# Performance work log

Measured on AMD Instinct MI355X. Metric: run time of the kernel, lower is better.

Reference implementation:

```python
import jax, jax.numpy as jnp
import numpy as np

B, S, D_MODEL = 2, 8192, 768
NUM_HEADS = 12
R = 4          # dilation_rate (= number of independent attention branches)
SEG = 512      # segment_size


def setup_inputs() -> dict:
    key = jax.random.key(0)
    ks = jax.random.split(key, 3)
    x = jax.random.normal(ks[0], (B, S, D_MODEL), jnp.float32)
    # Per-offset MHA weights: fused qkv proj and output proj (bias zeros)
    Wqkv = jax.random.normal(ks[1], (R, 3 * D_MODEL, D_MODEL), jnp.float32) * 0.02
    bqkv = jnp.zeros((R, 3 * D_MODEL), jnp.float32)
    Wout = jax.random.normal(ks[2], (R, D_MODEL, D_MODEL), jnp.float32) * 0.02
    bout = jnp.zeros((R, D_MODEL), jnp.float32)
    return {"x": x, "Wqkv": Wqkv, "bqkv": bqkv, "Wout": Wout, "bout": bout,
            "num_heads": NUM_HEADS}


def reference(x, Wqkv, bqkv, Wout, bout, num_heads):
    Bb, Ss, D = x.shape
    r = Wqkv.shape[0]
    L = Ss // r                # tokens per dilation offset
    n_seg = L // SEG           # segments per offset
    hd = D // num_heads

    # Dilated strided gather: x[:, o::r, :] for all offsets o -> (r, B, L, D)
    xo = jnp.moveaxis(x.reshape(Bb, L, r, D), 2, 0)

    # Per-offset fused qkv projection
    qkv = jnp.einsum('rbld,red->rble', xo, Wqkv) + bqkv[:, None, None, :]
    q, k, v = jnp.split(qkv, 3, axis=-1)
    seg = lambda t: t.reshape(r, Bb, n_seg, SEG, num_heads, hd)
    q, k, v = seg(q), seg(k), seg(v)  # (r, B, n_seg, SEG, H, hd)

    scale = 1.0 / np.sqrt(hd).astype(np.float32)
    scores = jnp.einsum('rbnqhd,rbnkhd->rbnhqk', q, k) * scale
    attn = jax.nn.softmax(scores, axis=-1)
    ctx = jnp.einsum('rbnhqk,rbnkhd->rbnqhd', attn, v).reshape(r, Bb, L, D)

    # Per-offset output projection
    out = jnp.einsum('rbld,red->rble', ctx, Wout) + bout[:, None, None, :]  # (r,B,L,D)

    # Scatter each offset's output back to its strided positions, zeros elsewhere,
    # then concat over offsets along the feature dim -> (B, S, r*D)
    res = jnp.zeros((Bb, Ss, r * D), x.dtype)
    for o in range(r):  # fixed small loop over dilation offsets
        res = res.at[:, o::r, o * D:(o + 1) * D].set(out[o])
    return res
```

## Files before the change

### kernel.cpp

```cpp
#include <hip/hip_runtime.h>

constexpr int Bb   = 2;
constexpr int S    = 8192;
constexpr int D    = 768;
constexpr int H    = 12;
constexpr int HD   = 64;
constexpr int R    = 4;
constexpr int L    = 2048;
constexpr int SEG  = 512;
constexpr int NSEG = 4;
constexpr int E3   = 3 * D;
constexpr int RD   = R * D;

typedef _Float16 f16x8 __attribute__((ext_vector_type(8)));
typedef _Float16 f16x4 __attribute__((ext_vector_type(4)));
typedef float    f32x4 __attribute__((ext_vector_type(4)));

#define AS1 __attribute__((address_space(1)))
#define AS3 __attribute__((address_space(3)))

__device__ __forceinline__ void gld16(const void* g, void* l) {
    __builtin_amdgcn_global_load_lds((AS1 void*)g, (AS3 void*)l, 16, 0, 0);
}

__global__ __launch_bounds__(256) void conv_one(const float4* __restrict__ x,
                                                f16x4* __restrict__ o, int n4)
{
    int i = blockIdx.x * 256 + threadIdx.x;
    const int stride = gridDim.x * 256;
    for (; i < n4; i += stride) {
        float4 v = x[i];
        f16x4 h;
        h[0] = (_Float16)v.x; h[1] = (_Float16)v.y;
        h[2] = (_Float16)v.z; h[3] = (_Float16)v.w;
        o[i] = h;
    }
}

template <int MODE>
__global__ __launch_bounds__(256) void mfma_gemm(const _Float16* __restrict__ Ah0,
                                                 const _Float16* __restrict__ Wh0,
                                                 const float* __restrict__ B0,
                                                 _Float16* __restrict__ Q0,
                                                 _Float16* __restrict__ K0,
                                                 _Float16* __restrict__ V0,
                                                 float* __restrict__ C0)
{
    constexpr int NXB = (MODE == 0) ? 18 : 6;
    constexpr int NWG = NXB * 16 * 8;
    const int wg = ((int)blockIdx.x & 7) * (NWG >> 3) + ((int)blockIdx.x >> 3);
    const int n0 = (wg % NXB) * 128;
    const int m0 = ((wg / NXB) & 15) * 128;
    const int z  = wg / (NXB * 16);
    const int r = z >> 1, b = z & 1;

    const _Float16* Ah; const _Float16* Wh; const float* bias;
    int lda;
    if (MODE == 0) {
        Ah = Ah0 + ((size_t)b * S + r) * D;  lda = RD;
        Wh = Wh0 + (size_t)r * E3 * D;
        bias = B0 + r * E3;
    } else {
        Ah = Ah0 + (size_t)z * L * D;        lda = D;
        Wh = Wh0 + (size_t)r * D * D;
        bias = B0 + r * D;
    }

    const int tid  = threadIdx.x;
    const int wave = tid >> 6;
    const int lane = tid & 63;
    const int lw   = lane & 15;
    const int quad = lane >> 4;
    const int wm   = wave & 1, wn = wave >> 1;

    __shared__ _Float16 sm[3][2][4096];

    f32x4 acc[4][4];
    #pragma unroll
    for (int mt = 0; mt < 4; mt++)
        #pragma unroll
        for (int nt = 0; nt < 4; nt++)
            acc[mt][nt] = f32x4{0.f, 0.f, 0.f, 0.f};

    const int srow = lane & 15;
    const int scol = (lane >> 4) * 8;

    auto stage = [&](int buf, int k0) {
        #pragma unroll
        for (int i = 0; i < 4; i++) {
            const int idx  = wave * 4 + i;
            const int tile = idx >> 3, g = idx & 7;
            const _Float16* src = (tile == 0) ? Ah : Wh;
            const int ldr   = (tile == 0) ? lda : D;
            const int base0 = (tile == 0) ? m0 : n0;
            gld16(src + (size_t)(base0 + g * 16 + srow) * ldr + k0 + scol,
                  &sm[buf][tile][g * 512]);
        }
    };

    stage(0, 0);
    stage(1, 32);

    for (int k = 0; k < 24; k++) {
        asm volatile("s_waitcnt lgkmcnt(0)" ::: "memory");
        if (k == 23) asm volatile("s_waitcnt vmcnt(0)" ::: "memory");
        else         asm volatile("s_waitcnt vmcnt(4)" ::: "memory");
        __builtin_amdgcn_s_barrier();
        __builtin_amdgcn_sched_barrier(0);

        const int buf = k % 3;
        f16x8 af[4], bf[4];
        #pragma unroll
        for (int mt = 0; mt < 4; mt++)
            af[mt] = *(const f16x8*)&sm[buf][0][(wm * 4 + mt) * 512 + quad * 128 + lw * 8];
        #pragma unroll
        for (int nt = 0; nt < 4; nt++)
            bf[nt] = *(const f16x8*)&sm[buf][1][(wn * 4 + nt) * 512 + quad * 128 + lw * 8];
        if (k + 2 < 24) stage((k + 2) % 3, (k + 2) * 32);
        #pragma unroll
        for (int mt = 0; mt < 4; mt++)
            #pragma unroll
            for (int nt = 0; nt < 4; nt++)
                acc[mt][nt] = __builtin_amdgcn_mfma_f32_16x16x32_f16(af[mt], bf[nt], acc[mt][nt], 0, 0, 0);
    }
    __syncthreads();

    float bv[4];
    #pragma unroll
    for (int nt = 0; nt < 4; nt++)
        bv[nt] = bias[n0 + wn * 64 + nt * 16 + lw];

    if (MODE == 0) {
        const int reg = n0 / D;
        if (reg < 2) {
            _Float16* G = (reg == 0 ? Q0 : K0) + (size_t)z * L * D;
            const int colbase = (n0 - reg * D) + wn * 64;
            _Float16* wbuf = &sm[0][0][wave * 2048];
            #pragma unroll
            for (int p = 0; p < 2; p++) {
                #pragma unroll
                for (int mtl = 0; mtl < 2; mtl++) {
                    const int mt = p * 2 + mtl;
                    #pragma unroll
                    for (int nt = 0; nt < 4; nt++)
                        #pragma unroll
                        for (int rr = 0; rr < 4; rr++)
                            wbuf[(mtl * 16 + quad * 4 + rr) * 64 + nt * 16 + lw] =
                                (_Float16)(acc[mt][nt][rr] + bv[nt]);
                }
                asm volatile("s_waitcnt lgkmcnt(0)" ::: "memory");
                #pragma unroll
                for (int j = 0; j < 4; j++) {
                    const int rl = (lane >> 3) + j * 8;
                    f16x8 v = *(const f16x8*)&wbuf[rl * 64 + (lane & 7) * 8];
                    const int l = m0 + wm * 64 + p * 32 + rl;
                    *(f16x8*)(G + (size_t)l * D + colbase + (lane & 7) * 8) = v;
                }
                asm volatile("s_waitcnt lgkmcnt(0)" ::: "memory");
            }
        } else {
            #pragma unroll
            for (int nt = 0; nt < 4; nt++) {
                const int e  = (n0 - 2 * D) + wn * 64 + nt * 16 + lw;
                const int hh = e >> 6, hd = e & 63;
                #pragma unroll
                for (int mt = 0; mt < 4; mt++) {
                    const int l = m0 + wm * 64 + mt * 16 + quad * 4;
                    const int ns = l >> 9, key = l & 511;
                    f16x4 v;
                    #pragma unroll
                    for (int rr = 0; rr < 4; rr++)
                        v[rr] = (_Float16)(acc[mt][nt][rr] + bv[nt]);
                    *(f16x4*)(V0 + ((size_t)((z * H + hh) * NSEG + ns)) * (HD * SEG)
                              + (size_t)hd * SEG + key) = v;
                }
            }
        }
    } else {
        float* Crow = C0 + (size_t)b * S * RD;
        #pragma unroll
        for (int mt = 0; mt < 4; mt++)
            #pragma unroll
            for (int nt = 0; nt < 4; nt++) {
                const int col = n0 + wn * 64 + nt * 16 + lw;
                #pragma unroll
                for (int rr = 0; rr < 4; rr++) {
                    const int l = m0 + wm * 64 + mt * 16 + quad * 4 + rr;
                    const float val = acc[mt][nt][rr] + bv[nt];
                    const size_t rowoff = (size_t)(l * R + r) * RD;
                    #pragma unroll
                    for (int rp = 0; rp < 4; rp++)
                        Crow[rowoff + rp * D + col] = (rp == r) ? val : 0.f;
                }
            }
    }
}

__global__ __launch_bounds__(256) void attn_mfma(const _Float16* __restrict__ Qh,
                                                 const _Float16* __restrict__ Kh,
                                                 const _Float16* __restrict__ Vt,
                                                 _Float16* __restrict__ ctx)
{
    __shared__ _Float16 Ks[3][4096];
    __shared__ _Float16 Vs[3][4096];
    __shared__ _Float16 Pw[16384];

    int t = ((int)blockIdx.x & 7) * 96 + ((int)blockIdx.x >> 3);
    const int qh = t & 1; t >>= 1;
    const int h  = t % H; t /= H;
    const int n  = t & 3; t >>= 2;
    const int z  = t;

    const int tid  = threadIdx.x;
    const int wave = tid >> 6;
    const int lane = tid & 63;
    const int lw   = lane & 15;
    const int quad = lane >> 4;
    const int srow = lane & 15;
    const int scol = (lane >> 4) * 8;

    const _Float16* Qg = Qh + ((size_t)(z * L + n * SEG + qh * 256)) * D + h * HD;
    #pragma unroll
    for (int i = 0; i < 8; i++) {
        const int qg = wave * 4 + (i >> 1), h2 = i & 1;
        gld16(Qg + (size_t)(qg * 16 + srow) * D + h2 * 32 + scol,
              &Pw[qg * 1024 + h2 * 512]);
    }
    __syncthreads();

    f16x8 qf[4][2];
    #pragma unroll
    for (int mt = 0; mt < 4; mt++)
        #pragma unroll
        for (int kk = 0; kk < 2; kk++)
            qf[mt][kk] = *(const f16x8*)&Pw[(wave * 4 + mt) * 1024 + (kk * 4 + quad) * 128 + lw * 8];

    const _Float16* Kg = Kh + ((size_t)(z * L + n * SEG)) * D + h * HD;
    const _Float16* Vg = Vt + ((size_t)((z * H + h) * NSEG + n)) * (HD * SEG);
    _Float16* Pv = Pw + wave * 4096;

    auto stageKV = [&](int buf, int kt) {
        #pragma unroll
        for (int i = 0; i < 4; i++) {
            const int idx = wave * 4 + i;
            const int j = idx & 7, g = j >> 1, h2 = j & 1;
            if (idx < 8)
                gld16(Kg + (size_t)(kt * 64 + g * 16 + srow) * D + h2 * 32 + scol,
                      &Ks[buf][g * 1024 + h2 * 512]);
            else
                gld16(Vg + (size_t)(g * 16 + srow) * SEG + kt * 64 + h2 * 32 + scol,
                      &Vs[buf][g * 1024 + h2 * 512]);
        }
    };

    f32x4 cacc[4][4];
    #pragma unroll
    for (int mt = 0; mt < 4; mt++)
        #pragma unroll
        for (int nt = 0; nt < 4; nt++)
            cacc[mt][nt] = f32x4{0.f, 0.f, 0.f, 0.f};
    float psum[4] = {0.f, 0.f, 0.f, 0.f};

    stageKV(0, 0);
    stageKV(1, 1);

    for (int kt = 0; kt < 8; kt++) {
        asm volatile("s_waitcnt lgkmcnt(0)" ::: "memory");
        if (kt == 7) asm volatile("s_waitcnt vmcnt(0)" ::: "memory");
        else         asm volatile("s_waitcnt vmcnt(4)" ::: "memory");
        __builtin_amdgcn_s_barrier();
        __builtin_amdgcn_sched_barrier(0);

        const int buf = kt % 3;
        if (kt + 2 < 8) stageKV((kt + 2) % 3, kt + 2);

        f32x4 Sc[4][4];
        #pragma unroll
        for (int mt = 0; mt < 4; mt++)
            #pragma unroll
            for (int nt = 0; nt < 4; nt++)
                Sc[mt][nt] = f32x4{0.f, 0.f, 0.f, 0.f};
        #pragma unroll
        for (int kk = 0; kk < 2; kk++)
            #pragma unroll
            for (int nt = 0; nt < 4; nt++) {
                f16x8 kf = *(const f16x8*)&Ks[buf][nt * 1024 + (kk * 4 + quad) * 128 + lw * 8];
                #pragma unroll
                for (int mt = 0; mt < 4; mt++)
                    Sc[mt][nt] = __builtin_amdgcn_mfma_f32_16x16x32_f16(kf, qf[mt][kk], Sc[mt][nt], 0, 0, 0);
            }

        #pragma unroll
        for (int mt = 0; mt < 4; mt++)
            #pragma unroll
            for (int nt = 0; nt < 4; nt++) {
                f16x4 p4;
                #pragma unroll
                for (int rr = 0; rr < 4; rr++)
                    p4[rr] = (_Float16)__expf(Sc[mt][nt][rr] * 0.125f);
                *(f16x4*)&Pv[mt * 1024 + (nt * 2 + (quad >> 1)) * 128 + lw * 8 + (quad & 1) * 4] = p4;
            }
        asm volatile("s_waitcnt lgkmcnt(0)" ::: "memory");

        #pragma unroll
        for (int kk = 0; kk < 2; kk++) {
            f16x8 pf[4], vf[4];
            #pragma unroll
            for (int mt = 0; mt < 4; mt++) {
                pf[mt] = *(const f16x8*)&Pv[mt * 1024 + (kk * 4 + quad) * 128 + lw * 8];
                float s = 0.f;
                #pragma unroll
                for (int j = 0; j < 8; j++) s += (float)pf[mt][j];
                psum[mt] += s;
            }
            #pragma unroll
            for (int nt = 0; nt < 4; nt++)
                vf[nt] = *(const f16x8*)&Vs[buf][nt * 1024 + (kk * 4 + quad) * 128 + lw * 8];
            #pragma unroll
            for (int mt = 0; mt < 4; mt++)
                #pragma unroll
                for (int nt = 0; nt < 4; nt++)
                    cacc[mt][nt] = __builtin_amdgcn_mfma_f32_16x16x32_f16(pf[mt], vf[nt], cacc[mt][nt], 0, 0, 0);
        }
    }

    #pragma unroll
    for (int mt = 0; mt < 4; mt++) {
        psum[mt] += __shfl_xor(psum[mt], 16);
        psum[mt] += __shfl_xor(psum[mt], 32);
    }
    _Float16* Cg = ctx + ((size_t)(z * L + n * SEG + qh * 256 + wave * 64)) * D + h * HD;
    #pragma unroll
    for (int mt = 0; mt < 4; mt++)
        #pragma unroll
        for (int rr = 0; rr < 4; rr++) {
            float iv = 1.0f / __shfl(psum[mt], quad * 4 + rr);
            int q = mt * 16 + quad * 4 + rr;
            #pragma unroll
            for (int nt = 0; nt < 4; nt++)
                Cg[(size_t)q * D + nt * 16 + lw] = (_Float16)(cacc[mt][nt][rr] * iv);
        }
}

extern "C" void kernel_launch(void* const* d_in, const int* in_sizes, int n_in,
                              void* d_out, int out_size, void* d_ws, size_t ws_size,
                              hipStream_t stream)
{
    const float* x    = (const float*)d_in[0];
    const float* Wqkv = (const float*)d_in[1];
    const float* bqkv = (const float*)d_in[2];
    const float* Wout = (const float*)d_in[3];
    const float* bout = (const float*)d_in[4];

    float* out = (float*)d_out;

    constexpr size_t NX   = (size_t)Bb * S * D;
    constexpr size_t NWQ  = (size_t)R * E3 * D;
    constexpr size_t NWO  = (size_t)R * D * D;
    constexpr size_t NTOK = (size_t)R * Bb * L;

    _Float16* Xh  = (_Float16*)d_ws;
    _Float16* Wqh = Xh  + NX;
    _Float16* Wo  = Wqh + NWQ;
    _Float16* Qh  = Wo  + NWO;
    _Float16* Kh  = Qh  + NTOK * D;
    _Float16* Vt  = Kh  + NTOK * D;
    _Float16* ctx = Vt  + NTOK * D;

    conv_one<<<2048, 256, 0, stream>>>((const float4*)x, (f16x4*)Xh, (int)(NX / 4));
    conv_one<<<2048, 256, 0, stream>>>((const float4*)Wqkv, (f16x4*)Wqh, (int)(NWQ / 4));
    conv_one<<<1024, 256, 0, stream>>>((const float4*)Wout, (f16x4*)Wo, (int)(NWO / 4));

    mfma_gemm<0><<<E3 / 128 * (L / 128) * R * Bb, 256, 0, stream>>>(
        Xh, Wqh, bqkv, Qh, Kh, Vt, nullptr);

    attn_mfma<<<R * Bb * NSEG * H * 2, 256, 0, stream>>>(Qh, Kh, Vt, ctx);

    mfma_gemm<1><<<D / 128 * (L / 128) * R * Bb, 256, 0, stream>>>(
        ctx, Wo, bout, nullptr, nullptr, nullptr, out);
}
```

Measured before the change: 465.6 us.

## Fuse conversion kernels, fold softmax scale into Q, use MFMA row sums and setprio

Merges the three fp32-to-fp16 conversion launches into one kernel. Folds the 1/sqrt(hd)*log2(e) factor into the Q projection epilogue so attention can use exp2 directly. Replaces the scalar per-lane probability summation and cross-lane shuffles with an extra MFMA against a ones vector. Raises wave priority around MFMA blocks in both the GEMM and attention kernels. These save launches and VALU work but add MFMA instructions and slightly change fp16 rounding of Q.

```diff
diff --git a/kernel.cpp b/kernel.cpp
--- a/kernel.cpp
+++ b/kernel.cpp
@@ -23,17 +23,26 @@
     __builtin_amdgcn_global_load_lds((AS1 void*)g, (AS3 void*)l, 16, 0, 0);
 }
 
-__global__ __launch_bounds__(256) void conv_one(const float4* __restrict__ x,
-                                                f16x4* __restrict__ o, int n4)
+__global__ __launch_bounds__(256) void conv_all(const float4* __restrict__ x,  f16x4* __restrict__ ox, int nx,
+                                                const float4* __restrict__ w1, f16x4* __restrict__ o1, int n1,
+                                                const float4* __restrict__ w2, f16x4* __restrict__ o2, int n2)
 {
-    int i = blockIdx.x * 256 + threadIdx.x;
     const int stride = gridDim.x * 256;
-    for (; i < n4; i += stride) {
+    const int t0 = blockIdx.x * 256 + threadIdx.x;
+    for (int i = t0; i < nx; i += stride) {
         float4 v = x[i];
-        f16x4 h;
-        h[0] = (_Float16)v.x; h[1] = (_Float16)v.y;
-        h[2] = (_Float16)v.z; h[3] = (_Float16)v.w;
-        o[i] = h;
+        f16x4 h; h[0]=(_Float16)v.x; h[1]=(_Float16)v.y; h[2]=(_Float16)v.z; h[3]=(_Float16)v.w;
+        ox[i] = h;
+    }
+    for (int i = t0; i < n1; i += stride) {
+        float4 v = w1[i];
+        f16x4 h; h[0]=(_Float16)v.x; h[1]=(_Float16)v.y; h[2]=(_Float16)v.z; h[3]=(_Float16)v.w;
+        o1[i] = h;
+    }
+    for (int i = t0; i < n2; i += stride) {
+        float4 v = w2[i];
+        f16x4 h; h[0]=(_Float16)v.x; h[1]=(_Float16)v.y; h[2]=(_Float16)v.z; h[3]=(_Float16)v.w;
+        o2[i] = h;
     }
 }
 
@@ -117,11 +126,13 @@
         for (int nt = 0; nt < 4; nt++)
             bf[nt] = *(const f16x8*)&sm[buf][1][(wn * 4 + nt) * 512 + quad * 128 + lw * 8];
         if (k + 2 < 24) stage((k + 2) % 3, (k + 2) * 32);
+        __builtin_amdgcn_s_setprio(1);
         #pragma unroll
         for (int mt = 0; mt < 4; mt++)
             #pragma unroll
             for (int nt = 0; nt < 4; nt++)
                 acc[mt][nt] = __builtin_amdgcn_mfma_f32_16x16x32_f16(af[mt], bf[nt], acc[mt][nt], 0, 0, 0);
+        __builtin_amdgcn_s_setprio(0);
     }
     __syncthreads();
 
@@ -133,6 +144,7 @@
     if (MODE == 0) {
         const int reg = n0 / D;
         if (reg < 2) {
+            const float qs = (reg == 0) ? 0.18033688011112042f : 1.0f;
             _Float16* G = (reg == 0 ? Q0 : K0) + (size_t)z * L * D;
             const int colbase = (n0 - reg * D) + wn * 64;
             _Float16* wbuf = &sm[0][0][wave * 2048];
@@ -146,7 +158,7 @@
                         #pragma unroll
                         for (int rr = 0; rr < 4; rr++)
                             wbuf[(mtl * 16 + quad * 4 + rr) * 64 + nt * 16 + lw] =
-                                (_Float16)(acc[mt][nt][rr] + bv[nt]);
+                                (_Float16)((acc[mt][nt][rr] + bv[nt]) * qs);
                 }
                 asm volatile("s_waitcnt lgkmcnt(0)" ::: "memory");
                 #pragma unroll
@@ -259,7 +271,13 @@
         #pragma unroll
         for (int nt = 0; nt < 4; nt++)
             cacc[mt][nt] = f32x4{0.f, 0.f, 0.f, 0.f};
-    float psum[4] = {0.f, 0.f, 0.f, 0.f};
+    f32x4 Ps[4];
+    #pragma unroll
+    for (int mt = 0; mt < 4; mt++)
+        Ps[mt] = f32x4{0.f, 0.f, 0.f, 0.f};
+    f16x8 ones;
+    #pragma unroll
+    for (int j = 0; j < 8; j++) ones[j] = (_Float16)1.0f;
 
     stageKV(0, 0);
     stageKV(1, 1);
@@ -280,6 +298,7 @@
             #pragma unroll
             for (int nt = 0; nt < 4; nt++)
                 Sc[mt][nt] = f32x4{0.f, 0.f, 0.f, 0.f};
+        __builtin_amdgcn_s_setprio(1);
         #pragma unroll
         for (int kk = 0; kk < 2; kk++)
             #pragma unroll
@@ -289,6 +308,7 @@
                 for (int mt = 0; mt < 4; mt++)
                     Sc[mt][nt] = __builtin_amdgcn_mfma_f32_16x16x32_f16(kf, qf[mt][kk], Sc[mt][nt], 0, 0, 0);
             }
+        __builtin_amdgcn_s_setprio(0);
 
         #pragma unroll
         for (int mt = 0; mt < 4; mt++)
@@ -297,44 +317,38 @@
                 f16x4 p4;
                 #pragma unroll
                 for (int rr = 0; rr < 4; rr++)
-                    p4[rr] = (_Float16)__expf(Sc[mt][nt][rr] * 0.125f);
+                    p4[rr] = (_Float16)exp2f(Sc[mt][nt][rr]);
                 *(f16x4*)&Pv[mt * 1024 + (nt * 2 + (quad >> 1)) * 128 + lw * 8 + (quad & 1) * 4] = p4;
             }
         asm volatile("s_waitcnt lgkmcnt(0)" ::: "memory");
 
+        __builtin_amdgcn_s_setprio(1);
         #pragma unroll
         for (int kk = 0; kk < 2; kk++) {
             f16x8 pf[4], vf[4];
             #pragma unroll
-            for (int mt = 0; mt < 4; mt++) {
+            for (int mt = 0; mt < 4; mt++)
                 pf[mt] = *(const f16x8*)&Pv[mt * 1024 + (kk * 4 + quad) * 128 + lw * 8];
-                float s = 0.f;
-                #pragma unroll
-                for (int j = 0; j < 8; j++) s += (float)pf[mt][j];
-                psum[mt] += s;
-            }
             #pragma unroll
             for (int nt = 0; nt < 4; nt++)
                 vf[nt] = *(const f16x8*)&Vs[buf][nt * 1024 + (kk * 4 + quad) * 128 + lw * 8];
             #pragma unroll
-            for (int mt = 0; mt < 4; mt++)
+            for (int mt = 0; mt < 4; mt++) {
+                Ps[mt] = __builtin_amdgcn_mfma_f32_16x16x32_f16(pf[mt], ones, Ps[mt], 0, 0, 0);
                 #pragma unroll
                 for (int nt = 0; nt < 4; nt++)
                     cacc[mt][nt] = __builtin_amdgcn_mfma_f32_16x16x32_f16(pf[mt], vf[nt], cacc[mt][nt], 0, 0, 0);
-        }
-    }
-
-    #pragma unroll
-    for (int mt = 0; mt < 4; mt++) {
-        psum[mt] += __shfl_xor(psum[mt], 16);
-        psum[mt] += __shfl_xor(psum[mt], 32);
-    }
+            }
+        }
+        __builtin_amdgcn_s_setprio(0);
+    }
+
     _Float16* Cg = ctx + ((size_t)(z * L + n * SEG + qh * 256 + wave * 64)) * D + h * HD;
     #pragma unroll
     for (int mt = 0; mt < 4; mt++)
         #pragma unroll
         for (int rr = 0; rr < 4; rr++) {
-            float iv = 1.0f / __shfl(psum[mt], quad * 4 + rr);
+            float iv = 1.0f / Ps[mt][rr];
             int q = mt * 16 + quad * 4 + rr;
             #pragma unroll
             for (int nt = 0; nt < 4; nt++)
@@ -367,9 +381,9 @@
     _Float16* Vt  = Kh  + NTOK * D;
     _Float16* ctx = Vt  + NTOK * D;
 
-    conv_one<<<2048, 256, 0, stream>>>((const float4*)x, (f16x4*)Xh, (int)(NX / 4));
-    conv_one<<<2048, 256, 0, stream>>>((const float4*)Wqkv, (f16x4*)Wqh, (int)(NWQ / 4));
-    conv_one<<<1024, 256, 0, stream>>>((const float4*)Wout, (f16x4*)Wo, (int)(NWO / 4));
+    conv_all<<<2048, 256, 0, stream>>>((const float4*)x,    (f16x4*)Xh,  (int)(NX / 4),
+                                       (const float4*)Wqkv, (f16x4*)Wqh, (int)(NWQ / 4),
+                                       (const float4*)Wout, (f16x4*)Wo,  (int)(NWO / 4));
 
     mfma_gemm<0><<<E3 / 128 * (L / 128) * R * Bb, 256, 0, stream>>>(
         Xh, Wqh, bqkv, Qh, Kh, Vt, nullptr);
```

Result: slower. 483.8 us (+3.9%).
